# Optimization experiments

Hardware: AMD Instinct MI355X
Metric: run time of the kernel (lower is better)

## Reference

```python
import jax, jax.numpy as jnp
import numpy as np

NUM_LABELS = 64  # number of distinct label ids (0 = background, unchanged)


def setup_inputs() -> dict:
    key = jax.random.key(0)
    k1, k2, k3 = jax.random.split(key, 3)
    shape = (2, 192, 256, 256)
    texturized = jax.random.normal(k1, shape, dtype=jnp.float32)
    label_map = jax.random.randint(k2, shape, 0, NUM_LABELS, dtype=jnp.int32)
    # one Uniform(0, intensity) draw per label, mirroring self.intensity() per loop iter
    intensities = jax.random.uniform(k3, (NUM_LABELS,), dtype=jnp.float32)
    return {"texturized": texturized, "label_map": label_map, "intensities": intensities}


def reference(texturized, label_map, intensities):
    # Per label l > 0 (torch loop): adjusted[mask_l] -= mean(tex[mask_l] - intensity_l)
    #                             = tex - (segment_mean_l - intensity_l) on mask_l.
    flat_tex = texturized.reshape(-1)
    flat_lab = label_map.reshape(-1)
    sums = jax.ops.segment_sum(flat_tex, flat_lab, num_segments=NUM_LABELS)
    counts = jax.ops.segment_sum(jnp.ones_like(flat_tex), flat_lab, num_segments=NUM_LABELS)
    means = sums / jnp.maximum(counts, 1.0)
    delta = means - intensities  # [NUM_LABELS] per-label bls.mean()
    adj = flat_tex - jnp.where(flat_lab > 0, delta[flat_lab], 0.0)
    return adj.reshape(texturized.shape)
```

## Files before the change

### kernel.cpp

```cpp
#include <hip/hip_runtime.h>
#include <stdint.h>

#define NL 64
#define NCOL 32

typedef float f32x4 __attribute__((ext_vector_type(4)));

static __device__ __forceinline__ void lds_add_f64(double* p, double v) {
    asm volatile("ds_add_f64 %0, %1"
                 :
                 : "v"((uint32_t)(uintptr_t)p), "v"(v)
                 : "memory");
}

__global__ __launch_bounds__(256, 8) void tl_reduce(const float* __restrict__ tex,
                                                    const int* __restrict__ lab,
                                                    float* __restrict__ g_sums,
                                                    unsigned int* __restrict__ g_cnts,
                                                    int n) {
    __shared__ double s_bin[NL * NCOL];
    __shared__ float s_s[256];
    __shared__ unsigned s_c[256];

    const int tid = threadIdx.x;
    const int col = tid & (NCOL - 1);

    for (int k = tid; k < NL * NCOL; k += 256) s_bin[k] = 0.0;
    __syncthreads();

    const int n4 = n >> 2;
    const float4* __restrict__ tex4 = (const float4*)tex;
    const int4* __restrict__ lab4 = (const int4*)lab;
    const int stride = gridDim.x * 256;

    int i = blockIdx.x * 256 + tid;
    bool vA = i < n4;
    bool vB = (i + stride) < n4;
    float4 tA, tB;
    int4 lA, lB;
    if (vA) { tA = tex4[i]; lA = lab4[i]; }
    if (vB) { tB = tex4[i + stride]; lB = lab4[i + stride]; }

    while (vA) {
        const int iC = i + 2 * stride;
        const bool vC = iC < n4;
        float4 tC;
        int4 lC;
        if (vC) { tC = tex4[iC]; lC = lab4[iC]; }

        lds_add_f64(&s_bin[((lA.x & (NL - 1)) << 5) | col], (double)tA.x + 4294967296.0);
        lds_add_f64(&s_bin[((lA.y & (NL - 1)) << 5) | col], (double)tA.y + 4294967296.0);
        lds_add_f64(&s_bin[((lA.z & (NL - 1)) << 5) | col], (double)tA.z + 4294967296.0);
        lds_add_f64(&s_bin[((lA.w & (NL - 1)) << 5) | col], (double)tA.w + 4294967296.0);

        tA = tB; lA = lB; vA = vB;
        tB = tC; lB = lC; vB = vC;
        i += stride;
    }

    if (blockIdx.x == 0) {
        const int base = n4 << 2;
        if (tid < n - base) {
            const int j = base + tid;
            lds_add_f64(&s_bin[((lab[j] & (NL - 1)) << 5) | col], (double)tex[j] + 4294967296.0);
        }
    }
    __syncthreads();

    {
        const int l = tid >> 2, q = tid & 3;
        double v = 0.0;
#pragma unroll
        for (int j = 0; j < 8; ++j) v += s_bin[(l << 5) | (q << 3) | j];
        const double ci = floor(v * (1.0 / 4294967296.0) + 0.5);
        s_s[tid] = (float)(v - ci * 4294967296.0);
        s_c[tid] = (unsigned)ci;
    }
    __syncthreads();

    if (tid < NL) {
        const int b = tid << 2;
        atomicAdd(&g_sums[tid], s_s[b] + s_s[b + 1] + s_s[b + 2] + s_s[b + 3]);
        atomicAdd(&g_cnts[tid], s_c[b] + s_c[b + 1] + s_c[b + 2] + s_c[b + 3]);
    }
}

__global__ __launch_bounds__(256, 8) void tl_apply(const float* __restrict__ tex,
                                                   const int* __restrict__ lab,
                                                   const float* __restrict__ g_sums,
                                                   const unsigned int* __restrict__ g_cnts,
                                                   const float* __restrict__ intens,
                                                   float* __restrict__ out, int n) {
    __shared__ float s_delta[NL];
    if (threadIdx.x < NL) {
        const int l = threadIdx.x;
        const float mean = g_sums[l] / fmaxf((float)g_cnts[l], 1.0f);
        s_delta[l] = (l > 0) ? (mean - intens[l]) : 0.0f;
    }
    __syncthreads();

    const int tid = threadIdx.x;
    const int n4 = n >> 2;
    const float4* __restrict__ tex4 = (const float4*)tex;
    const int4* __restrict__ lab4 = (const int4*)lab;
    float4* __restrict__ out4 = (float4*)out;
    const int stride = gridDim.x * 256;

    int i = blockIdx.x * 256 + tid;
    bool vA = i < n4;
    bool vB = (i + stride) < n4;
    float4 tA, tB;
    int4 lA, lB;
    if (vA) { tA = tex4[i]; lA = lab4[i]; }
    if (vB) { tB = tex4[i + stride]; lB = lab4[i + stride]; }

    while (vA) {
        const int iC = i + 2 * stride;
        const bool vC = iC < n4;
        float4 tC;
        int4 lC;
        if (vC) { tC = tex4[iC]; lC = lab4[iC]; }

        float4 o;
        o.x = tA.x - s_delta[lA.x & (NL - 1)];
        o.y = tA.y - s_delta[lA.y & (NL - 1)];
        o.z = tA.z - s_delta[lA.z & (NL - 1)];
        o.w = tA.w - s_delta[lA.w & (NL - 1)];
        __builtin_nontemporal_store(*(const f32x4*)&o, (f32x4*)&out4[i]);

        tA = tB; lA = lB; vA = vB;
        tB = tC; lB = lC; vB = vC;
        i += stride;
    }

    if (blockIdx.x == 0) {
        const int base = n4 << 2;
        if (tid < n - base) {
            const int j = base + tid;
            out[j] = tex[j] - s_delta[lab[j] & (NL - 1)];
        }
    }
}

extern "C" void kernel_launch(void* const* d_in, const int* in_sizes, int n_in,
                              void* d_out, int out_size, void* d_ws, size_t ws_size,
                              hipStream_t stream) {
    const float* tex    = (const float*)d_in[0];
    const int*   lab    = (const int*)d_in[1];
    const float* intens = (const float*)d_in[2];
    float* out = (float*)d_out;
    const int n = in_sizes[0];

    float* g_sums = (float*)d_ws;
    unsigned int* g_cnts = (unsigned int*)((char*)d_ws + NL * sizeof(float));

    hipMemsetAsync(d_ws, 0, NL * (sizeof(float) + sizeof(unsigned int)), stream);

    tl_reduce<<<2048, 256, 0, stream>>>(tex, lab, g_sums, g_cnts, n);

    tl_apply<<<4096, 256, 0, stream>>>(tex, lab, g_sums, g_cnts, intens, out, n);
}
```

Measured before the change: 301.9 us.

## Fuse reduce and apply into one persistent kernel with grid barrier

Merges the histogram-reduce and apply kernels into a single persistent kernel of single-wave blocks, synchronised by a global atomic spin barrier. Each lane owns a private column of 64 double bins, so LDS atomics become plain read-modify-write adds, and the prefetch depth goes from two to three stages. This removes one launch and the LDS atomic cost, but it relies on all 1024 blocks being co-resident for the barrier and uses far fewer threads per CU, which may lower memory-level parallelism.

```diff
diff --git a/kernel.cpp b/kernel.cpp
--- a/kernel.cpp
+++ b/kernel.cpp
@@ -2,59 +2,55 @@
 #include <stdint.h>
 
 #define NL 64
-#define NCOL 32
+#define NBLOCKS 1024
 
 typedef float f32x4 __attribute__((ext_vector_type(4)));
 
-static __device__ __forceinline__ void lds_add_f64(double* p, double v) {
-    asm volatile("ds_add_f64 %0, %1"
-                 :
-                 : "v"((uint32_t)(uintptr_t)p), "v"(v)
-                 : "memory");
-}
-
-__global__ __launch_bounds__(256, 8) void tl_reduce(const float* __restrict__ tex,
-                                                    const int* __restrict__ lab,
-                                                    float* __restrict__ g_sums,
-                                                    unsigned int* __restrict__ g_cnts,
-                                                    int n) {
-    __shared__ double s_bin[NL * NCOL];
-    __shared__ float s_s[256];
-    __shared__ unsigned s_c[256];
+__global__ __launch_bounds__(64) void tl_fused(const float* __restrict__ tex,
+                                               const int* __restrict__ lab,
+                                               float* __restrict__ g_sums,
+                                               unsigned int* __restrict__ g_cnts,
+                                               unsigned int* __restrict__ g_bar,
+                                               const float* __restrict__ intens,
+                                               float* __restrict__ out, int n) {
+    __shared__ double bins[NL * 64];
 
     const int tid = threadIdx.x;
-    const int col = tid & (NCOL - 1);
 
-    for (int k = tid; k < NL * NCOL; k += 256) s_bin[k] = 0.0;
+    #pragma unroll
+    for (int j = 0; j < NL; ++j) bins[j * 64 + tid] = 0.0;
     __syncthreads();
 
     const int n4 = n >> 2;
     const float4* __restrict__ tex4 = (const float4*)tex;
     const int4* __restrict__ lab4 = (const int4*)lab;
-    const int stride = gridDim.x * 256;
+    const int stride = gridDim.x * 64;
 
-    int i = blockIdx.x * 256 + tid;
+    int i = blockIdx.x * 64 + tid;
     bool vA = i < n4;
     bool vB = (i + stride) < n4;
-    float4 tA, tB;
-    int4 lA, lB;
+    bool vC = (i + 2 * stride) < n4;
+    float4 tA, tB, tC;
+    int4 lA, lB, lC;
     if (vA) { tA = tex4[i]; lA = lab4[i]; }
     if (vB) { tB = tex4[i + stride]; lB = lab4[i + stride]; }
+    if (vC) { tC = tex4[i + 2 * stride]; lC = lab4[i + 2 * stride]; }
 
     while (vA) {
-        const int iC = i + 2 * stride;
-        const bool vC = iC < n4;
-        float4 tC;
-        int4 lC;
-        if (vC) { tC = tex4[iC]; lC = lab4[iC]; }
+        const int iD = i + 3 * stride;
+        const bool vD = iD < n4;
+        float4 tD;
+        int4 lD;
+        if (vD) { tD = tex4[iD]; lD = lab4[iD]; }
 
-        lds_add_f64(&s_bin[((lA.x & (NL - 1)) << 5) | col], (double)tA.x + 4294967296.0);
-        lds_add_f64(&s_bin[((lA.y & (NL - 1)) << 5) | col], (double)tA.y + 4294967296.0);
-        lds_add_f64(&s_bin[((lA.z & (NL - 1)) << 5) | col], (double)tA.z + 4294967296.0);
-        lds_add_f64(&s_bin[((lA.w & (NL - 1)) << 5) | col], (double)tA.w + 4294967296.0);
+        bins[((lA.x & (NL - 1)) << 6) | tid] += (double)tA.x + 4294967296.0;
+        bins[((lA.y & (NL - 1)) << 6) | tid] += (double)tA.y + 4294967296.0;
+        bins[((lA.z & (NL - 1)) << 6) | tid] += (double)tA.z + 4294967296.0;
+        bins[((lA.w & (NL - 1)) << 6) | tid] += (double)tA.w + 4294967296.0;
 
         tA = tB; lA = lB; vA = vB;
         tB = tC; lB = lC; vB = vC;
+        tC = tD; lC = lD; vC = vD;
         i += stride;
     }
 
@@ -62,64 +58,57 @@
         const int base = n4 << 2;
         if (tid < n - base) {
             const int j = base + tid;
-            lds_add_f64(&s_bin[((lab[j] & (NL - 1)) << 5) | col], (double)tex[j] + 4294967296.0);
+            bins[((lab[j] & (NL - 1)) << 6) | tid] += (double)tex[j] + 4294967296.0;
         }
     }
     __syncthreads();
 
     {
-        const int l = tid >> 2, q = tid & 3;
         double v = 0.0;
-#pragma unroll
-        for (int j = 0; j < 8; ++j) v += s_bin[(l << 5) | (q << 3) | j];
+        #pragma unroll
+        for (int j = 0; j < 64; ++j) v += bins[(tid << 6) | ((tid + j) & 63)];
         const double ci = floor(v * (1.0 / 4294967296.0) + 0.5);
-        s_s[tid] = (float)(v - ci * 4294967296.0);
-        s_c[tid] = (unsigned)ci;
+        const float bsum = (float)(v - ci * 4294967296.0);
+        atomicAdd(&g_sums[tid], bsum);
+        atomicAdd(&g_cnts[tid], (unsigned int)ci);
+    }
+
+    __threadfence();
+    if (tid == 0) {
+        __hip_atomic_fetch_add(g_bar, 1u, __ATOMIC_ACQ_REL, __HIP_MEMORY_SCOPE_AGENT);
+        while (__hip_atomic_load(g_bar, __ATOMIC_ACQUIRE, __HIP_MEMORY_SCOPE_AGENT) <
+               (unsigned int)gridDim.x) {
+            __builtin_amdgcn_s_sleep(8);
+        }
     }
     __syncthreads();
 
-    if (tid < NL) {
-        const int b = tid << 2;
-        atomicAdd(&g_sums[tid], s_s[b] + s_s[b + 1] + s_s[b + 2] + s_s[b + 3]);
-        atomicAdd(&g_cnts[tid], s_c[b] + s_c[b + 1] + s_c[b + 2] + s_c[b + 3]);
-    }
-}
-
-__global__ __launch_bounds__(256, 8) void tl_apply(const float* __restrict__ tex,
-                                                   const int* __restrict__ lab,
-                                                   const float* __restrict__ g_sums,
-                                                   const unsigned int* __restrict__ g_cnts,
-                                                   const float* __restrict__ intens,
-                                                   float* __restrict__ out, int n) {
-    __shared__ float s_delta[NL];
-    if (threadIdx.x < NL) {
-        const int l = threadIdx.x;
-        const float mean = g_sums[l] / fmaxf((float)g_cnts[l], 1.0f);
-        s_delta[l] = (l > 0) ? (mean - intens[l]) : 0.0f;
+    float* s_delta = (float*)bins;
+    {
+        const float ss = __hip_atomic_load(&g_sums[tid], __ATOMIC_RELAXED,
+                                           __HIP_MEMORY_SCOPE_AGENT);
+        const unsigned int cc = __hip_atomic_load(&g_cnts[tid], __ATOMIC_RELAXED,
+                                                  __HIP_MEMORY_SCOPE_AGENT);
+        const float mean = ss / fmaxf((float)cc, 1.0f);
+        s_delta[tid] = (tid > 0) ? (mean - intens[tid]) : 0.0f;
     }
     __syncthreads();
 
-    const int tid = threadIdx.x;
-    const int n4 = n >> 2;
-    const float4* __restrict__ tex4 = (const float4*)tex;
-    const int4* __restrict__ lab4 = (const int4*)lab;
     float4* __restrict__ out4 = (float4*)out;
-    const int stride = gridDim.x * 256;
-
-    int i = blockIdx.x * 256 + tid;
-    bool vA = i < n4;
-    bool vB = (i + stride) < n4;
-    float4 tA, tB;
-    int4 lA, lB;
+    i = blockIdx.x * 64 + tid;
+    vA = i < n4;
+    vB = (i + stride) < n4;
+    vC = (i + 2 * stride) < n4;
     if (vA) { tA = tex4[i]; lA = lab4[i]; }
     if (vB) { tB = tex4[i + stride]; lB = lab4[i + stride]; }
+    if (vC) { tC = tex4[i + 2 * stride]; lC = lab4[i + 2 * stride]; }
 
     while (vA) {
-        const int iC = i + 2 * stride;
-        const bool vC = iC < n4;
-        float4 tC;
-        int4 lC;
-        if (vC) { tC = tex4[iC]; lC = lab4[iC]; }
+        const int iD = i + 3 * stride;
+        const bool vD = iD < n4;
+        float4 tD;
+        int4 lD;
+        if (vD) { tD = tex4[iD]; lD = lab4[iD]; }
 
         float4 o;
         o.x = tA.x - s_delta[lA.x & (NL - 1)];
@@ -130,6 +119,7 @@
 
         tA = tB; lA = lB; vA = vB;
         tB = tC; lB = lC; vB = vC;
+        tC = tD; lC = lD; vC = vD;
         i += stride;
     }
 
@@ -152,11 +142,10 @@
     const int n = in_sizes[0];
 
     float* g_sums = (float*)d_ws;
-    unsigned int* g_cnts = (unsigned int*)((char*)d_ws + NL * sizeof(float));
+    unsigned int* g_cnts = (unsigned int*)((char*)d_ws + 256);
+    unsigned int* g_bar  = (unsigned int*)((char*)d_ws + 512);
+    hipMemsetAsync(d_ws, 0, 1024, stream);
 
-    hipMemsetAsync(d_ws, 0, NL * (sizeof(float) + sizeof(unsigned int)), stream);
-
-    tl_reduce<<<2048, 256, 0, stream>>>(tex, lab, g_sums, g_cnts, n);
-
-    tl_apply<<<4096, 256, 0, stream>>>(tex, lab, g_sums, g_cnts, intens, out, n);
+    tl_fused<<<NBLOCKS, 64, 0, stream>>>(tex, lab, g_sums, g_cnts, g_bar,
+                                         intens, out, n);
 }
```

After: 367.1 us. 1.22x slower.
